# Optimization experiments

Hardware: AMD Instinct MI355X
Metric: run time of the kernel (lower is better)

The kernel has to match this reference:

```python
import jax, jax.numpy as jnp
import numpy as np

H = 16
D_MODEL = 1024
D_HEAD = D_MODEL // H  # 64


def _xavier(key, shape):
    # xavier_uniform over last two dims (matches torch init on [h, in, out])
    fan_in, fan_out = shape[-2], shape[-1]
    limit = float(np.sqrt(6.0 / (fan_in + fan_out)))
    return jax.random.uniform(key, shape, jnp.float32, -limit, limit)


def setup_inputs() -> dict:
    key = jax.random.key(0)
    ks = jax.random.split(key, 7)
    B, S = 4, 2048
    x_q = jax.random.normal(ks[0], (B, S, D_MODEL), jnp.float32)
    x_k = jax.random.normal(ks[1], (B, S, D_MODEL), jnp.float32)
    x_v = jax.random.normal(ks[2], (B, S, D_MODEL), jnp.float32)
    W_Q = _xavier(ks[3], (H, D_MODEL, D_HEAD))
    W_K = _xavier(ks[4], (H, D_MODEL, D_HEAD))
    W_V = _xavier(ks[5], (H, D_MODEL, D_HEAD))
    # torch Linear weight: [out_features, in_features], y = x @ W^T
    lim = float(np.sqrt(6.0 / (2 * D_MODEL)))  # kaiming-uniform-ish default approximated by xavier for reproducibility
    W_O = jax.random.uniform(ks[6], (D_MODEL, D_MODEL), jnp.float32, -lim, lim)
    return {"x_q": x_q, "x_k": x_k, "x_v": x_v,
            "W_Q": W_Q, "W_K": W_K, "W_V": W_V, "W_O": W_O}


def reference(x_q, x_k, x_v, W_Q, W_K, W_V, W_O):
    d_scale = jnp.asarray(D_HEAD, jnp.float32) ** 0.25  # d_q == d_k == dim_q**(1/4)
    # per-head projections: [b,s,m] x [h,m,d] -> [b,h,s,d]
    Q = jnp.einsum('bsm,hmd->bhsd', x_q, W_Q)
    K = jnp.einsum('bsm,hmd->bhsd', x_k, W_K)
    V = jnp.einsum('bsm,hmd->bhsd', x_v, W_V)
    # column softmax over K^T: shape [b,h,d,s], softmax over dim=-2 (the d axis)
    Kt = jnp.swapaxes(K, -1, -2) / d_scale          # [b,h,d,s]
    Kt = jax.nn.softmax(Kt, axis=-2)
    A = jnp.einsum('bhds,bhse->bhde', Kt, V)        # KV precompute [b,h,d,d]
    Qs = jax.nn.softmax(Q / d_scale, axis=-1)       # row softmax over head dim
    Bt = jnp.einsum('bhsd,bhde->bhse', Qs, A)       # [b,h,s,d]
    b, h, s, d = Bt.shape
    # faithful to torch .view on contiguous [b,h,s,d] -> [b,s,h*d] (pure reshape, no transpose)
    Bt = Bt.reshape(b, s, h * d)
    return jnp.einsum('bsi,oi->bso', Bt, W_O)
```

## Files before the change

kernel.cpp:

```cpp
#include <hip/hip_runtime.h>
#include <cstdint>
#include <cstddef>

#define DMODEL 1024
#define HEADS  16
#define DHEAD  64
#define BATCH  4
#define SEQ    2048
#define ROWS   (BATCH * SEQ)
#define INV_DSCALE 0.3535533905932738f

typedef float  f32x4  __attribute__((ext_vector_type(4)));
typedef __bf16 bf16x8 __attribute__((ext_vector_type(8)));
typedef unsigned short u16x8 __attribute__((ext_vector_type(8)));

__device__ __forceinline__ unsigned short f2bf(float x) {
    union { float f; unsigned u; } c; c.f = x;
    unsigned u = c.u;
    return (unsigned short)((u + 0x7fffu + ((u >> 16) & 1u)) >> 16);
}

__device__ __forceinline__ unsigned cvt_pk_bf16(float a, float b) {
#if __has_builtin(__builtin_amdgcn_cvt_pk_bf16_f32)
    typedef __bf16 bf16x2_t __attribute__((ext_vector_type(2)));
    union { bf16x2_t v; unsigned u; } c;
    c.v = __builtin_amdgcn_cvt_pk_bf16_f32(a, b);
    return c.u;
#else
    return (unsigned)f2bf(a) | ((unsigned)f2bf(b) << 16);
#endif
}

__device__ __forceinline__ void load_g2l16(const unsigned short* g, unsigned short* l) {
    __builtin_amdgcn_global_load_lds(
        (const __attribute__((address_space(1))) unsigned int*)g,
        (__attribute__((address_space(3))) unsigned int*)l,
        16 , 0 , 0 );
}

__global__ __launch_bounds__(256) void prep_w(const float* __restrict__ W0,
                                              const float* __restrict__ W1,
                                              const float* __restrict__ W2,
                                              const float* __restrict__ Wo,
                                              unsigned short* __restrict__ T0,
                                              unsigned short* __restrict__ T1,
                                              unsigned short* __restrict__ T2,
                                              unsigned short* __restrict__ To) {
    __shared__ float tile[64][68];
    int blk = blockIdx.x;
    int t = threadIdx.x;
    if (blk < 768) {
        int w = blk >> 8, h = (blk >> 4) & 15, mb = blk & 15;
        const float* W = w == 0 ? W0 : (w == 1 ? W1 : W2);
        unsigned short* T = w == 0 ? T0 : (w == 1 ? T1 : T2);
        #pragma unroll
        for (int i = 0; i < 4; ++i) {
            int f = t + 256 * i;
            int m = f >> 4, dg = (f & 15) * 4;
            *(float4*)&tile[m][dg] = *(const float4*)&W[((size_t)(h * 16 + mb) * 64 + m) * 64 + dg];
        }
        __syncthreads();
        #pragma unroll
        for (int i = 0; i < 2; ++i) {
            int f = t + 256 * i;
            int d = f >> 3, mg = f & 7;
            ushort4 a, b;
            a.x = f2bf(tile[mg * 8 + 0][d]); a.y = f2bf(tile[mg * 8 + 1][d]);
            a.z = f2bf(tile[mg * 8 + 2][d]); a.w = f2bf(tile[mg * 8 + 3][d]);
            b.x = f2bf(tile[mg * 8 + 4][d]); b.y = f2bf(tile[mg * 8 + 5][d]);
            b.z = f2bf(tile[mg * 8 + 6][d]); b.w = f2bf(tile[mg * 8 + 7][d]);
            unsigned short* dst = T + (size_t)(h * 64 + d) * DMODEL + mb * 64 + mg * 8;
            *(ushort4*)dst = a; *(ushort4*)(dst + 4) = b;
        }
    } else {
        int i = (blk - 768) * 256 + t;
        float4 v = ((const float4*)Wo)[i];
        ushort4 o;
        o.x = f2bf(v.x); o.y = f2bf(v.y); o.z = f2bf(v.z); o.w = f2bf(v.w);
        ((ushort4*)To)[i] = o;
    }
}

template <bool AF32>
__device__ __forceinline__ void gemm_tile(const void* __restrict__ Av,
                                          const unsigned short* __restrict__ Bp,
                                          int K, int bm0, int bn0,
                                          unsigned short* smem, f32x4 acc[2][4]) {
    unsigned short* ldsA = smem;
    unsigned short* ldsB = smem + 4096;

    const int t    = threadIdx.x;
    const int lane = t & 63;
    const int wave = t >> 6;
    const int wm   = (wave & 1) * 32;
    const int wn   = (wave >> 1) * 64;
    const int fr   = lane & 15;
    const int quad = lane >> 4;

    const float*          A32 = (const float*)Av;
    const unsigned short* A16 = (const unsigned short*)Av;

    unsigned offA[2], offB[4];
    #pragma unroll
    for (int i = 0; i < 2; ++i) {
        int f = t + 256 * i, row = f >> 3, kg = (f & 7) ^ (row & 7);
        offA[i] = (unsigned)(bm0 + row) * K + kg * 8;
    }
    #pragma unroll
    for (int i = 0; i < 4; ++i) {
        int f = t + 256 * i, row = f >> 3, kg = (f & 7) ^ (row & 7);
        offB[i] = (unsigned)(bn0 + row) * K + kg * 8;
    }

    for (int k0 = 0; k0 < K; k0 += 64) {
        if (AF32) {
            #pragma unroll
            for (int i = 0; i < 2; ++i) {
                const float* src = A32 + offA[i] + k0;
                float4 lo = *(const float4*)src;
                float4 hi = *(const float4*)(src + 4);
                uint4 pk;
                pk.x = cvt_pk_bf16(lo.x, lo.y);
                pk.y = cvt_pk_bf16(lo.z, lo.w);
                pk.z = cvt_pk_bf16(hi.x, hi.y);
                pk.w = cvt_pk_bf16(hi.z, hi.w);
                *(uint4*)&ldsA[(t + 256 * i) * 8] = pk;
            }
        } else {
            #pragma unroll
            for (int i = 0; i < 2; ++i)
                load_g2l16(A16 + offA[i] + k0, &ldsA[(t + 256 * i) * 8]);
        }
        #pragma unroll
        for (int i = 0; i < 4; ++i)
            load_g2l16(Bp + offB[i] + k0, &ldsB[(t + 256 * i) * 8]);
        asm volatile("s_waitcnt vmcnt(0)" ::: "memory");
        __syncthreads();

        bf16x8 af[2][2], bfr[4][2];
        #pragma unroll
        for (int i = 0; i < 2; ++i) {
            int row = wm + i * 16 + fr;
            #pragma unroll
            for (int kh = 0; kh < 2; ++kh) {
                int s = (kh * 4 + quad) ^ (row & 7);
                af[i][kh] = *reinterpret_cast<const bf16x8*>(&ldsA[row * 64 + s * 8]);
            }
        }
        #pragma unroll
        for (int j = 0; j < 4; ++j) {
            int row = wn + j * 16 + fr;
            #pragma unroll
            for (int kh = 0; kh < 2; ++kh) {
                int s = (kh * 4 + quad) ^ (row & 7);
                bfr[j][kh] = *reinterpret_cast<const bf16x8*>(&ldsB[row * 64 + s * 8]);
            }
        }
        #pragma unroll
        for (int kh = 0; kh < 2; ++kh)
            #pragma unroll
            for (int i = 0; i < 2; ++i)
                #pragma unroll
                for (int j = 0; j < 4; ++j)
                    acc[i][j] = __builtin_amdgcn_mfma_f32_16x16x32_bf16(af[i][kh], bfr[j][kh], acc[i][j], 0, 0, 0);

        __syncthreads();
    }
}

__device__ __forceinline__ void softmax4(float v[4]) {
    #pragma unroll
    for (int j = 0; j < 4; ++j) v[j] *= INV_DSCALE;
    float m = fmaxf(fmaxf(v[0], v[1]), fmaxf(v[2], v[3]));
    #pragma unroll
    for (int off = 8; off; off >>= 1) m = fmaxf(m, __shfl_xor(m, off, 16));
    float s = 0.f;
    #pragma unroll
    for (int j = 0; j < 4; ++j) { v[j] = __expf(v[j] - m); s += v[j]; }
    #pragma unroll
    for (int off = 8; off; off >>= 1) s += __shfl_xor(s, off, 16);
    float inv = 1.0f / s;
    #pragma unroll
    for (int j = 0; j < 4; ++j) v[j] *= inv;
}

__device__ __forceinline__ void decode_blk(int flat, int& bm0, int& bn0) {
    int xcd = flat & 7, idx = flat >> 3;
    bm0 = (xcd * 16 + (idx >> 3)) * 64;
    bn0 = (idx & 7) * 128;
}

__global__ __launch_bounds__(256, 4) void proj3(const float* __restrict__ xq,
                                                const float* __restrict__ xk,
                                                const float* __restrict__ xv,
                                                const unsigned short* __restrict__ wq,
                                                const unsigned short* __restrict__ wk,
                                                const unsigned short* __restrict__ wv,
                                                unsigned short* __restrict__ Qb,
                                                unsigned short* __restrict__ Kt,
                                                unsigned short* __restrict__ Vt) {
    __shared__ unsigned short smem[12288];
    int z = blockIdx.y;
    const float* A = z == 0 ? xq : (z == 1 ? xk : xv);
    const unsigned short* B = z == 0 ? wq : (z == 1 ? wk : wv);
    int bm0, bn0;
    decode_blk(blockIdx.x, bm0, bn0);

    f32x4 acc[2][4] = {};
    gemm_tile<true>(A, B, DMODEL, bm0, bn0, smem, acc);

    const int t    = threadIdx.x;
    const int lane = t & 63;
    const int wave = t >> 6;
    const int wm   = (wave & 1) * 32;
    const int wn   = (wave >> 1) * 64;
    const int fr   = lane & 15;
    const int quad = lane >> 4;
    bool do_sm = (z < 2);

    if (z == 0) {
        #pragma unroll
        for (int i = 0; i < 2; ++i)
            #pragma unroll
            for (int r = 0; r < 4; ++r) {
                float v[4];
                #pragma unroll
                for (int j = 0; j < 4; ++j) v[j] = acc[i][j][r];
                softmax4(v);
                int rr = bm0 + wm + i * 16 + quad * 4 + r;
                size_t base = (size_t)rr * DMODEL + bn0 + wn + fr;
                #pragma unroll
                for (int j = 0; j < 4; ++j) Qb[base + j * 16] = f2bf(v[j]);
            }
    } else {
        unsigned short* Ct = smem;
        #pragma unroll
        for (int i = 0; i < 2; ++i)
            #pragma unroll
            for (int r = 0; r < 4; ++r) {
                float v[4];
                #pragma unroll
                for (int j = 0; j < 4; ++j) v[j] = acc[i][j][r];
                if (do_sm) softmax4(v);
                int rr = wm + i * 16 + quad * 4 + r;
                #pragma unroll
                for (int j = 0; j < 4; ++j) {
                    int cc = wn + j * 16 + fr;
                    Ct[cc * 72 + rr] = f2bf(v[j]);
                }
            }
        __syncthreads();
        unsigned short* T = (z == 1) ? Kt : Vt;
        int c = t >> 1, sh = (t & 1) * 32;
        int col = bn0 + c, h = col >> 6, d = col & 63;
        int b = bm0 >> 11, s0 = bm0 & 2047;
        unsigned short* dst = T + (((size_t)(b * 16 + h) * 64 + d) << 11) + s0 + sh;
        const unsigned short* src = &Ct[c * 72 + sh];
        #pragma unroll
        for (int k = 0; k < 4; ++k)
            *(uint4*)(dst + k * 8) = *(const uint4*)(src + k * 8);
    }
}

__global__ __launch_bounds__(256, 4) void gemm_out(const unsigned short* __restrict__ R,
                                                   const unsigned short* __restrict__ Wo,
                                                   float* __restrict__ out) {
    __shared__ unsigned short smem[12288];
    int bm0, bn0;
    decode_blk(blockIdx.x, bm0, bn0);
    f32x4 acc[2][4] = {};
    gemm_tile<false>(R, Wo, DMODEL, bm0, bn0, smem, acc);

    const int t = threadIdx.x, lane = t & 63, wave = t >> 6;
    const int wm = (wave & 1) * 32, wn = (wave >> 1) * 64;
    const int fr = lane & 15, quad = lane >> 4;
    #pragma unroll
    for (int i = 0; i < 2; ++i)
        #pragma unroll
        for (int r = 0; r < 4; ++r) {
            int rr = bm0 + wm + i * 16 + quad * 4 + r;
            size_t base = (size_t)rr * DMODEL + bn0 + wn + fr;
            #pragma unroll
            for (int j = 0; j < 4; ++j) out[base + j * 16] = acc[i][j][r];
        }
}

__global__ __launch_bounds__(256) void kv_mfma(const unsigned short* __restrict__ Vt,
                                               const unsigned short* __restrict__ Kt,
                                               float* __restrict__ P) {
    __shared__ unsigned short ldsV[64 * 64];
    __shared__ unsigned short ldsK[64 * 64];
    int bh = blockIdx.x >> 3, chunk = blockIdx.x & 7;
    int t = threadIdx.x, lane = t & 63, wave = t >> 6;
    int fr = lane & 15, quad = lane >> 4;

    unsigned offV[2], offK[2];
    #pragma unroll
    for (int i = 0; i < 2; ++i) {
        int f = t + 256 * i, row = f >> 3, kg = (f & 7) ^ (row & 7);
        unsigned o = ((unsigned)(bh * 64 + row) << 11) + chunk * 256 + kg * 8;
        offV[i] = o; offK[i] = o;
    }

    f32x4 acc[4] = {};
    for (int k0 = 0; k0 < 256; k0 += 64) {
        #pragma unroll
        for (int i = 0; i < 2; ++i)
            load_g2l16(Vt + offV[i] + k0, &ldsV[(t + 256 * i) * 8]);
        #pragma unroll
        for (int i = 0; i < 2; ++i)
            load_g2l16(Kt + offK[i] + k0, &ldsK[(t + 256 * i) * 8]);
        asm volatile("s_waitcnt vmcnt(0)" ::: "memory");
        __syncthreads();

        #pragma unroll
        for (int kh = 0; kh < 2; ++kh) {
            int rowA = wave * 16 + fr;
            int sA = (kh * 4 + quad) ^ (rowA & 7);
            bf16x8 av = *reinterpret_cast<const bf16x8*>(&ldsV[rowA * 64 + sA * 8]);
            #pragma unroll
            for (int j = 0; j < 4; ++j) {
                int rowB = j * 16 + fr;
                int sB = (kh * 4 + quad) ^ (rowB & 7);
                bf16x8 bv = *reinterpret_cast<const bf16x8*>(&ldsK[rowB * 64 + sB * 8]);
                acc[j] = __builtin_amdgcn_mfma_f32_16x16x32_bf16(av, bv, acc[j], 0, 0, 0);
            }
        }
        __syncthreads();
    }
    float* Pp = P + ((size_t)chunk * 64 + bh) * 4096;
    #pragma unroll
    for (int j = 0; j < 4; ++j)
        #pragma unroll
        for (int r = 0; r < 4; ++r)
            Pp[(wave * 16 + quad * 4 + r) * 64 + j * 16 + fr] = acc[j][r];
}

__global__ __launch_bounds__(256) void reduce_A(const float* __restrict__ P,
                                                unsigned short* __restrict__ At) {
    int idx = blockIdx.x * 256 + threadIdx.x;
    float s = 0.f;
    #pragma unroll
    for (int c = 0; c < 8; ++c) s += P[(size_t)c * (64 * 4096) + idx];
    At[idx] = f2bf(s);
}

__global__ __launch_bounds__(256, 4) void qs_mfma(const unsigned short* __restrict__ Qb,
                                                  const unsigned short* __restrict__ At,
                                                  unsigned short* __restrict__ R) {
    __shared__ unsigned short ldsQ[128 * 64];
    __shared__ unsigned short ldsB[64 * 64];
    int bh = blockIdx.x >> 4, sb = blockIdx.x & 15;
    int b = bh >> 4, h = bh & 15;
    int t = threadIdx.x, lane = t & 63, wave = t >> 6;
    int fr = lane & 15, quad = lane >> 4;
    int wm = wave * 32;

    #pragma unroll
    for (int i = 0; i < 4; ++i) {
        int f = t + 256 * i, row = f >> 3, kg = (f & 7) ^ (row & 7);
        const unsigned short* src = Qb + ((size_t)(b * SEQ + sb * 128 + row) << 10) + h * 64 + kg * 8;
        load_g2l16(src, &ldsQ[f * 8]);
    }
    #pragma unroll
    for (int i = 0; i < 2; ++i) {
        int f = t + 256 * i, row = f >> 3, kg = (f & 7) ^ (row & 7);
        load_g2l16(At + (unsigned)bh * 4096 + row * 64 + kg * 8, &ldsB[f * 8]);
    }
    asm volatile("s_waitcnt vmcnt(0)" ::: "memory");
    __syncthreads();

    f32x4 acc[2][4] = {};
    #pragma unroll
    for (int kh = 0; kh < 2; ++kh) {
        bf16x8 af[2], bfr[4];
        #pragma unroll
        for (int i = 0; i < 2; ++i) {
            int row = wm + i * 16 + fr;
            int s = (kh * 4 + quad) ^ (row & 7);
            af[i] = *reinterpret_cast<const bf16x8*>(&ldsQ[row * 64 + s * 8]);
        }
        #pragma unroll
        for (int j = 0; j < 4; ++j) {
            int row = j * 16 + fr;
            int s = (kh * 4 + quad) ^ (row & 7);
            bfr[j] = *reinterpret_cast<const bf16x8*>(&ldsB[row * 64 + s * 8]);
        }
        #pragma unroll
        for (int i = 0; i < 2; ++i)
            #pragma unroll
            for (int j = 0; j < 4; ++j)
                acc[i][j] = __builtin_amdgcn_mfma_f32_16x16x32_bf16(af[i], bfr[j], acc[i][j], 0, 0, 0);
    }

    #pragma unroll
    for (int i = 0; i < 2; ++i)
        #pragma unroll
        for (int r = 0; r < 4; ++r) {
            int rr = wm + i * 16 + quad * 4 + r;
            size_t base = ((size_t)bh << 17) + (size_t)(sb * 128 + rr) * 64;
            #pragma unroll
            for (int j = 0; j < 4; ++j)
                R[base + j * 16 + fr] = f2bf(acc[i][j][r]);
        }
}

extern "C" void kernel_launch(void* const* d_in, const int* in_sizes, int n_in,
                              void* d_out, int out_size, void* d_ws, size_t ws_size,
                              hipStream_t stream) {
    const float* xq = (const float*)d_in[0];
    const float* xk = (const float*)d_in[1];
    const float* xv = (const float*)d_in[2];
    const float* Wq = (const float*)d_in[3];
    const float* Wk = (const float*)d_in[4];
    const float* Wv = (const float*)d_in[5];
    const float* Wo = (const float*)d_in[6];
    float* out = (float*)d_out;
    char* ws = (char*)d_ws;

    const size_t MB = 1ull << 20;
    unsigned short* wq_t = (unsigned short*)(ws + 0 * MB);
    unsigned short* wk_t = (unsigned short*)(ws + 2 * MB);
    unsigned short* wv_t = (unsigned short*)(ws + 4 * MB);
    unsigned short* wo_b = (unsigned short*)(ws + 6 * MB);
    unsigned short* Qb = (unsigned short*)(ws + 8 * MB);
    unsigned short* Kt = (unsigned short*)(ws + 24 * MB);
    unsigned short* Vt = (unsigned short*)(ws + 40 * MB);
    unsigned short* At = (unsigned short*)(ws + 56 * MB);
    unsigned short* R  = (unsigned short*)(ws + 57 * MB);
    float* P = (float*)(ws + 73 * MB);

    prep_w<<<1792, 256, 0, stream>>>(Wq, Wk, Wv, Wo, wq_t, wk_t, wv_t, wo_b);

    proj3<<<dim3(1024, 3), 256, 0, stream>>>(xq, xk, xv, wq_t, wk_t, wv_t, Qb, Kt, Vt);

    kv_mfma<<<BATCH * HEADS * 8, 256, 0, stream>>>(Vt, Kt, P);
    reduce_A<<<1024, 256, 0, stream>>>(P, At);

    qs_mfma<<<BATCH * HEADS * 16, 256, 0, stream>>>(Qb, At, R);

    gemm_out<<<1024, 256, 0, stream>>>(R, wo_b, out);
}
```

Measured before the change: 269.0 us.

## Enlarge projection GEMM tile to 128x128 with 32-wide K steps

The fused Q/K/V projection kernel now computes 128x128 output tiles per block instead of 64x128. Each wave holds a 4x4 MFMA accumulator grid, the K loop steps by 32 with a 4-way XOR swizzle, and the grid is halved. This doubles reuse of each staged B tile and cuts redundant loads of the fp32 activations. In exchange it raises register pressure, lowers occupancy (launch bounds 4 to 3), uses a larger LDS transpose buffer, and adds more barrier iterations per block.

New measurement: 275.0 us. +2.2%, slower.

```diff
diff --git a/kernel.cpp b/kernel.cpp
--- a/kernel.cpp
+++ b/kernel.cpp
@@ -36,6 +36,22 @@
         (const __attribute__((address_space(1))) unsigned int*)g,
         (__attribute__((address_space(3))) unsigned int*)l,
         16 , 0 , 0 );
+}
+
+__device__ __forceinline__ void softmax4(float v[4]) {
+    #pragma unroll
+    for (int j = 0; j < 4; ++j) v[j] *= INV_DSCALE;
+    float m = fmaxf(fmaxf(v[0], v[1]), fmaxf(v[2], v[3]));
+    #pragma unroll
+    for (int off = 8; off; off >>= 1) m = fmaxf(m, __shfl_xor(m, off, 16));
+    float s = 0.f;
+    #pragma unroll
+    for (int j = 0; j < 4; ++j) { v[j] = __expf(v[j] - m); s += v[j]; }
+    #pragma unroll
+    for (int off = 8; off; off >>= 1) s += __shfl_xor(s, off, 16);
+    float inv = 1.0f / s;
+    #pragma unroll
+    for (int j = 0; j < 4; ++j) v[j] *= inv;
 }
 
 __global__ __launch_bounds__(256) void prep_w(const float* __restrict__ W0,
@@ -81,116 +97,7 @@
     }
 }
 
-template <bool AF32>
-__device__ __forceinline__ void gemm_tile(const void* __restrict__ Av,
-                                          const unsigned short* __restrict__ Bp,
-                                          int K, int bm0, int bn0,
-                                          unsigned short* smem, f32x4 acc[2][4]) {
-    unsigned short* ldsA = smem;
-    unsigned short* ldsB = smem + 4096;
-
-    const int t    = threadIdx.x;
-    const int lane = t & 63;
-    const int wave = t >> 6;
-    const int wm   = (wave & 1) * 32;
-    const int wn   = (wave >> 1) * 64;
-    const int fr   = lane & 15;
-    const int quad = lane >> 4;
-
-    const float*          A32 = (const float*)Av;
-    const unsigned short* A16 = (const unsigned short*)Av;
-
-    unsigned offA[2], offB[4];
-    #pragma unroll
-    for (int i = 0; i < 2; ++i) {
-        int f = t + 256 * i, row = f >> 3, kg = (f & 7) ^ (row & 7);
-        offA[i] = (unsigned)(bm0 + row) * K + kg * 8;
-    }
-    #pragma unroll
-    for (int i = 0; i < 4; ++i) {
-        int f = t + 256 * i, row = f >> 3, kg = (f & 7) ^ (row & 7);
-        offB[i] = (unsigned)(bn0 + row) * K + kg * 8;
-    }
-
-    for (int k0 = 0; k0 < K; k0 += 64) {
-        if (AF32) {
-            #pragma unroll
-            for (int i = 0; i < 2; ++i) {
-                const float* src = A32 + offA[i] + k0;
-                float4 lo = *(const float4*)src;
-                float4 hi = *(const float4*)(src + 4);
-                uint4 pk;
-                pk.x = cvt_pk_bf16(lo.x, lo.y);
-                pk.y = cvt_pk_bf16(lo.z, lo.w);
-                pk.z = cvt_pk_bf16(hi.x, hi.y);
-                pk.w = cvt_pk_bf16(hi.z, hi.w);
-                *(uint4*)&ldsA[(t + 256 * i) * 8] = pk;
-            }
-        } else {
-            #pragma unroll
-            for (int i = 0; i < 2; ++i)
-                load_g2l16(A16 + offA[i] + k0, &ldsA[(t + 256 * i) * 8]);
-        }
-        #pragma unroll
-        for (int i = 0; i < 4; ++i)
-            load_g2l16(Bp + offB[i] + k0, &ldsB[(t + 256 * i) * 8]);
-        asm volatile("s_waitcnt vmcnt(0)" ::: "memory");
-        __syncthreads();
-
-        bf16x8 af[2][2], bfr[4][2];
-        #pragma unroll
-        for (int i = 0; i < 2; ++i) {
-            int row = wm + i * 16 + fr;
-            #pragma unroll
-            for (int kh = 0; kh < 2; ++kh) {
-                int s = (kh * 4 + quad) ^ (row & 7);
-                af[i][kh] = *reinterpret_cast<const bf16x8*>(&ldsA[row * 64 + s * 8]);
-            }
-        }
-        #pragma unroll
-        for (int j = 0; j < 4; ++j) {
-            int row = wn + j * 16 + fr;
-            #pragma unroll
-            for (int kh = 0; kh < 2; ++kh) {
-                int s = (kh * 4 + quad) ^ (row & 7);
-                bfr[j][kh] = *reinterpret_cast<const bf16x8*>(&ldsB[row * 64 + s * 8]);
-            }
-        }
-        #pragma unroll
-        for (int kh = 0; kh < 2; ++kh)
-            #pragma unroll
-            for (int i = 0; i < 2; ++i)
-                #pragma unroll
-                for (int j = 0; j < 4; ++j)
-                    acc[i][j] = __builtin_amdgcn_mfma_f32_16x16x32_bf16(af[i][kh], bfr[j][kh], acc[i][j], 0, 0, 0);
-
-        __syncthreads();
-    }
-}
-
-__device__ __forceinline__ void softmax4(float v[4]) {
-    #pragma unroll
-    for (int j = 0; j < 4; ++j) v[j] *= INV_DSCALE;
-    float m = fmaxf(fmaxf(v[0], v[1]), fmaxf(v[2], v[3]));
-    #pragma unroll
-    for (int off = 8; off; off >>= 1) m = fmaxf(m, __shfl_xor(m, off, 16));
-    float s = 0.f;
-    #pragma unroll
-    for (int j = 0; j < 4; ++j) { v[j] = __expf(v[j] - m); s += v[j]; }
-    #pragma unroll
-    for (int off = 8; off; off >>= 1) s += __shfl_xor(s, off, 16);
-    float inv = 1.0f / s;
-    #pragma unroll
-    for (int j = 0; j < 4; ++j) v[j] *= inv;
-}
-
-__device__ __forceinline__ void decode_blk(int flat, int& bm0, int& bn0) {
-    int xcd = flat & 7, idx = flat >> 3;
-    bm0 = (xcd * 16 + (idx >> 3)) * 64;
-    bn0 = (idx & 7) * 128;
-}
-
-__global__ __launch_bounds__(256, 4) void proj3(const float* __restrict__ xq,
+__global__ __launch_bounds__(256, 3) void proj3(const float* __restrict__ xq,
                                                 const float* __restrict__ xk,
                                                 const float* __restrict__ xv,
                                                 const unsigned short* __restrict__ wq,
@@ -199,28 +106,81 @@
                                                 unsigned short* __restrict__ Qb,
                                                 unsigned short* __restrict__ Kt,
                                                 unsigned short* __restrict__ Vt) {
-    __shared__ unsigned short smem[12288];
+    __shared__ unsigned short smem[17408];
+    unsigned short* ldsA = smem;
+    unsigned short* ldsB = smem + 4096;
+
     int z = blockIdx.y;
     const float* A = z == 0 ? xq : (z == 1 ? xk : xv);
     const unsigned short* B = z == 0 ? wq : (z == 1 ? wk : wv);
-    int bm0, bn0;
-    decode_blk(blockIdx.x, bm0, bn0);
-
-    f32x4 acc[2][4] = {};
-    gemm_tile<true>(A, B, DMODEL, bm0, bn0, smem, acc);
+
+    int flat = blockIdx.x;
+    int xcd = flat & 7, idx = flat >> 3;
+    int bm0 = (xcd * 8 + (idx >> 3)) * 128;
+    int bn0 = (idx & 7) * 128;
 
     const int t    = threadIdx.x;
     const int lane = t & 63;
     const int wave = t >> 6;
-    const int wm   = (wave & 1) * 32;
+    const int wm   = (wave & 1) * 64;
     const int wn   = (wave >> 1) * 64;
     const int fr   = lane & 15;
     const int quad = lane >> 4;
-    bool do_sm = (z < 2);
+
+    f32x4 acc[4][4] = {};
+
+    unsigned offA[2], offB[2];
+    #pragma unroll
+    for (int i = 0; i < 2; ++i) {
+        int f = t + 256 * i, row = f >> 2, kg = (f & 3) ^ (row & 3);
+        offA[i] = (unsigned)(bm0 + row) * DMODEL + kg * 8;
+        offB[i] = (unsigned)(bn0 + row) * DMODEL + kg * 8;
+    }
+
+    for (int k0 = 0; k0 < DMODEL; k0 += 32) {
+        #pragma unroll
+        for (int i = 0; i < 2; ++i) {
+            const float* src = A + offA[i] + k0;
+            float4 lo = *(const float4*)src;
+            float4 hi = *(const float4*)(src + 4);
+            uint4 pk;
+            pk.x = cvt_pk_bf16(lo.x, lo.y);
+            pk.y = cvt_pk_bf16(lo.z, lo.w);
+            pk.z = cvt_pk_bf16(hi.x, hi.y);
+            pk.w = cvt_pk_bf16(hi.z, hi.w);
+            *(uint4*)&ldsA[(t + 256 * i) * 8] = pk;
+        }
+        #pragma unroll
+        for (int i = 0; i < 2; ++i)
+            load_g2l16(B + offB[i] + k0, &ldsB[(t + 256 * i) * 8]);
+        asm volatile("s_waitcnt vmcnt(0)" ::: "memory");
+        __syncthreads();
+
+        bf16x8 af[4], bfr[4];
+        #pragma unroll
+        for (int i = 0; i < 4; ++i) {
+            int row = wm + i * 16 + fr;
+            int s = quad ^ (row & 3);
+            af[i] = *reinterpret_cast<const bf16x8*>(&ldsA[row * 32 + s * 8]);
+        }
+        #pragma unroll
+        for (int j = 0; j < 4; ++j) {
+            int row = wn + j * 16 + fr;
+            int s = quad ^ (row & 3);
+            bfr[j] = *reinterpret_cast<const bf16x8*>(&ldsB[row * 32 + s * 8]);
+        }
+        #pragma unroll
+        for (int i = 0; i < 4; ++i)
+            #pragma unroll
+            for (int j = 0; j < 4; ++j)
+                acc[i][j] = __builtin_amdgcn_mfma_f32_16x16x32_bf16(af[i], bfr[j], acc[i][j], 0, 0, 0);
+
+        __syncthreads();
+    }
 
     if (z == 0) {
         #pragma unroll
-        for (int i = 0; i < 2; ++i)
+        for (int i = 0; i < 4; ++i)
             #pragma unroll
             for (int r = 0; r < 4; ++r) {
                 float v[4];
@@ -235,31 +195,105 @@
     } else {
         unsigned short* Ct = smem;
         #pragma unroll
-        for (int i = 0; i < 2; ++i)
+        for (int i = 0; i < 4; ++i)
             #pragma unroll
             for (int r = 0; r < 4; ++r) {
                 float v[4];
                 #pragma unroll
                 for (int j = 0; j < 4; ++j) v[j] = acc[i][j][r];
-                if (do_sm) softmax4(v);
+                if (z == 1) softmax4(v);
                 int rr = wm + i * 16 + quad * 4 + r;
                 #pragma unroll
                 for (int j = 0; j < 4; ++j) {
                     int cc = wn + j * 16 + fr;
-                    Ct[cc * 72 + rr] = f2bf(v[j]);
+                    Ct[cc * 136 + rr] = f2bf(v[j]);
                 }
             }
         __syncthreads();
         unsigned short* T = (z == 1) ? Kt : Vt;
-        int c = t >> 1, sh = (t & 1) * 32;
+        int c = t >> 1, sh = (t & 1) * 64;
         int col = bn0 + c, h = col >> 6, d = col & 63;
         int b = bm0 >> 11, s0 = bm0 & 2047;
         unsigned short* dst = T + (((size_t)(b * 16 + h) * 64 + d) << 11) + s0 + sh;
-        const unsigned short* src = &Ct[c * 72 + sh];
-        #pragma unroll
-        for (int k = 0; k < 4; ++k)
+        const unsigned short* src = &Ct[c * 136 + sh];
+        #pragma unroll
+        for (int k = 0; k < 8; ++k)
             *(uint4*)(dst + k * 8) = *(const uint4*)(src + k * 8);
     }
+}
+
+__device__ __forceinline__ void gemm_tile_out(const unsigned short* __restrict__ Ap,
+                                              const unsigned short* __restrict__ Bp,
+                                              int K, int bm0, int bn0,
+                                              unsigned short* smem, f32x4 acc[2][4]) {
+    unsigned short* ldsA = smem;
+    unsigned short* ldsB = smem + 4096;
+
+    const int t    = threadIdx.x;
+    const int lane = t & 63;
+    const int wave = t >> 6;
+    const int wm   = (wave & 1) * 32;
+    const int wn   = (wave >> 1) * 64;
+    const int fr   = lane & 15;
+    const int quad = lane >> 4;
+
+    unsigned offA[2], offB[4];
+    #pragma unroll
+    for (int i = 0; i < 2; ++i) {
+        int f = t + 256 * i, row = f >> 3, kg = (f & 7) ^ (row & 7);
+        offA[i] = (unsigned)(bm0 + row) * K + kg * 8;
+    }
+    #pragma unroll
+    for (int i = 0; i < 4; ++i) {
+        int f = t + 256 * i, row = f >> 3, kg = (f & 7) ^ (row & 7);
+        offB[i] = (unsigned)(bn0 + row) * K + kg * 8;
+    }
+
+    for (int k0 = 0; k0 < K; k0 += 64) {
+        #pragma unroll
+        for (int i = 0; i < 2; ++i)
+            load_g2l16(Ap + offA[i] + k0, &ldsA[(t + 256 * i) * 8]);
+        #pragma unroll
+        for (int i = 0; i < 4; ++i)
+            load_g2l16(Bp + offB[i] + k0, &ldsB[(t + 256 * i) * 8]);
+        asm volatile("s_waitcnt vmcnt(0)" ::: "memory");
+        __syncthreads();
+
+        bf16x8 af[2][2], bfr[4][2];
+        #pragma unroll
+        for (int i = 0; i < 2; ++i) {
+            int row = wm + i * 16 + fr;
+            #pragma unroll
+            for (int kh = 0; kh < 2; ++kh) {
+                int s = (kh * 4 + quad) ^ (row & 7);
+                af[i][kh] = *reinterpret_cast<const bf16x8*>(&ldsA[row * 64 + s * 8]);
+            }
+        }
+        #pragma unroll
+        for (int j = 0; j < 4; ++j) {
+            int row = wn + j * 16 + fr;
+            #pragma unroll
+            for (int kh = 0; kh < 2; ++kh) {
+                int s = (kh * 4 + quad) ^ (row & 7);
+                bfr[j][kh] = *reinterpret_cast<const bf16x8*>(&ldsB[row * 64 + s * 8]);
+            }
+        }
+        #pragma unroll
+        for (int kh = 0; kh < 2; ++kh)
+            #pragma unroll
+            for (int i = 0; i < 2; ++i)
+                #pragma unroll
+                for (int j = 0; j < 4; ++j)
+                    acc[i][j] = __builtin_amdgcn_mfma_f32_16x16x32_bf16(af[i][kh], bfr[j][kh], acc[i][j], 0, 0, 0);
+
+        __syncthreads();
+    }
+}
+
+__device__ __forceinline__ void decode_blk64(int flat, int& bm0, int& bn0) {
+    int xcd = flat & 7, idx = flat >> 3;
+    bm0 = (xcd * 16 + (idx >> 3)) * 64;
+    bn0 = (idx & 7) * 128;
 }
 
 __global__ __launch_bounds__(256, 4) void gemm_out(const unsigned short* __restrict__ R,
@@ -267,9 +301,9 @@
                                                    float* __restrict__ out) {
     __shared__ unsigned short smem[12288];
     int bm0, bn0;
-    decode_blk(blockIdx.x, bm0, bn0);
+    decode_blk64(blockIdx.x, bm0, bn0);
     f32x4 acc[2][4] = {};
-    gemm_tile<false>(R, Wo, DMODEL, bm0, bn0, smem, acc);
+    gemm_tile_out(R, Wo, DMODEL, bm0, bn0, smem, acc);
 
     const int t = threadIdx.x, lane = t & 63, wave = t >> 6;
     const int wm = (wave & 1) * 32, wn = (wave >> 1) * 64;
@@ -432,7 +466,7 @@
 
     prep_w<<<1792, 256, 0, stream>>>(Wq, Wk, Wv, Wo, wq_t, wk_t, wv_t, wo_b);
 
-    proj3<<<dim3(1024, 3), 256, 0, stream>>>(xq, xk, xv, wq_t, wk_t, wv_t, Qb, Kt, Vt);
+    proj3<<<dim3(512, 3), 256, 0, stream>>>(xq, xk, xv, wq_t, wk_t, wv_t, Qb, Kt, Vt);
 
     kv_mfma<<<BATCH * HEADS * 8, 256, 0, stream>>>(Vt, Kt, P);
     reduce_A<<<1024, 256, 0, stream>>>(P, At);
```
